# Kernel tuning notes

Measured on AMD Instinct MI355X. Metric: run time of the kernel, lower is better.

Reference implementation:

```python
import jax, jax.numpy as jnp
import numpy as np

B, S, D = 4, 4096, 64

def setup_inputs() -> dict:
    key = jax.random.key(0)
    k1, k2, k3 = jax.random.split(key, 3)
    inputs = jax.random.normal(k1, (B, S, D), dtype=jnp.float32)
    rotation = jax.random.normal(k2, (D, D), dtype=jnp.float32)
    entangle = jax.random.normal(k3, (D, D), dtype=jnp.float32)
    return {"inputs": inputs, "rotation": rotation, "entangle": entangle}

def reference(inputs, rotation, entangle):
    # query/key projections: [B,S,D] @ [D,D] -> [B,S,D]
    query = jnp.einsum('bsd,de->bse', inputs, rotation)
    key = jnp.einsum('bsd,de->bse', inputs, entangle)
    scale = 1.0 / jnp.sqrt(jnp.float32(inputs.shape[-1]))
    # scores: [B,S,S] softmax over last axis
    scores = jax.nn.softmax(jnp.einsum('bqd,bkd->bqk', query, key) * scale, axis=-1)
    # values are the raw inputs (no value projection)
    return jnp.einsum('bqk,bkd->bqd', scores, inputs)
```

## Files before the change

kernel.cpp:

```cpp
#include <hip/hip_runtime.h>
#include <hip/hip_fp16.h>

#define BB 4
#define SS 4096
#define DD 64
#define NSPLIT 8
#define KT_PER (SS / 64 / NSPLIT)

typedef _Float16 half8 __attribute__((ext_vector_type(8)));
typedef _Float16 half4 __attribute__((ext_vector_type(4)));
typedef __fp16 fp16x2 __attribute__((ext_vector_type(2)));
typedef float floatx4 __attribute__((ext_vector_type(4)));

__global__ __launch_bounds__(256) void proj_kernel(
    const float* __restrict__ X, const float* __restrict__ R, const float* __restrict__ E,
    _Float16* __restrict__ Qhi, _Float16* __restrict__ Qlo,
    _Float16* __restrict__ Khi, _Float16* __restrict__ Klo,
    _Float16* __restrict__ Vt)
{
    __shared__ float Rs[64][64];
    __shared__ float Es[64][64];
    __shared__ float Xs[16][68];
    int t = threadIdx.x;
    long rowbase = (long)blockIdx.x * 16;

    for (int j = 0; j < 4; ++j) {
        int idx = j * 256 + t;
        int r = idx >> 4;
        int c = (idx & 15) * 4;
        *(float4*)&Rs[r][c] = ((const float4*)R)[idx];
        *(float4*)&Es[r][c] = ((const float4*)E)[idx];
    }
    *(float4*)&Xs[t >> 4][(t & 15) * 4] = ((const float4*)(X + rowbase * 64))[t];
    __syncthreads();

    int row = t >> 4;
    int c0 = (t & 15) * 4;
    float q[4] = {0.f, 0.f, 0.f, 0.f}, k[4] = {0.f, 0.f, 0.f, 0.f};
#pragma unroll 4
    for (int d = 0; d < 64; ++d) {
        float x = Xs[row][d];
        float4 rv = *(const float4*)&Rs[d][c0];
        float4 ev = *(const float4*)&Es[d][c0];
        q[0] = fmaf(x, rv.x, q[0]); q[1] = fmaf(x, rv.y, q[1]);
        q[2] = fmaf(x, rv.z, q[2]); q[3] = fmaf(x, rv.w, q[3]);
        k[0] = fmaf(x, ev.x, k[0]); k[1] = fmaf(x, ev.y, k[1]);
        k[2] = fmaf(x, ev.z, k[2]); k[3] = fmaf(x, ev.w, k[3]);
    }
    long gq = (rowbase + row) * 64 + c0;
    half4 qh, ql, kh, kl;
#pragma unroll
    for (int j = 0; j < 4; ++j) {
        _Float16 h = (_Float16)q[j];
        qh[j] = h; ql[j] = (_Float16)(q[j] - (float)h);
        h = (_Float16)k[j];
        kh[j] = h; kl[j] = (_Float16)(k[j] - (float)h);
    }
    *(half4*)(Qhi + gq) = qh; *(half4*)(Qlo + gq) = ql;
    *(half4*)(Khi + gq) = kh; *(half4*)(Klo + gq) = kl;

    int d = t >> 2;
    int si = (t & 3) * 4;
    int b = (int)(rowbase >> 12);
    int sbase = (int)(rowbase & 4095);
    half4 v;
#pragma unroll
    for (int j = 0; j < 4; ++j) v[j] = (_Float16)Xs[si + j][d];
    *(half4*)(Vt + ((long)(b * 64 + d)) * SS + sbase + si) = v;
}

#define L2E 1.44269504088896340736f

__device__ __forceinline__ void glds16(const _Float16* g, _Float16* l) {
    __builtin_amdgcn_global_load_lds(
        (const __attribute__((address_space(1))) unsigned*)g,
        (__attribute__((address_space(3))) unsigned*)l, 16, 0, 0);
}

__global__ __launch_bounds__(128, 3) void attn_partial(
    const _Float16* __restrict__ Qhi, const _Float16* __restrict__ Qlo,
    const _Float16* __restrict__ Khi, const _Float16* __restrict__ Klo,
    const _Float16* __restrict__ Vt,
    float* __restrict__ Op, float* __restrict__ Mp, float* __restrict__ Lp)
{
    __shared__ _Float16 Ksh[64 * 64];
    __shared__ _Float16 Ksl[64 * 64];
    __shared__ _Float16 Ps[2 * 32 * 64];

    int t = threadIdx.x;
    int wave = t >> 6;
    int lane = t & 63;
    int l15 = lane & 15;
    int quad = lane >> 4;
    int split = blockIdx.y;
    int b = blockIdx.z;
    int q0 = blockIdx.x * 64 + wave * 32;

    half8 qah0, qah1, qbh0, qbh1, qal0, qal1, qbl0, qbl1;
    {
        long qrow = ((long)b * SS + q0 + l15) * DD;
        qah0 = *(const half8*)(Qhi + qrow + quad * 8);
        qah1 = *(const half8*)(Qhi + qrow + 32 + quad * 8);
        qal0 = *(const half8*)(Qlo + qrow + quad * 8);
        qal1 = *(const half8*)(Qlo + qrow + 32 + quad * 8);
        long qrow2 = qrow + 16 * DD;
        qbh0 = *(const half8*)(Qhi + qrow2 + quad * 8);
        qbh1 = *(const half8*)(Qhi + qrow2 + 32 + quad * 8);
        qbl0 = *(const half8*)(Qlo + qrow2 + quad * 8);
        qbl1 = *(const half8*)(Qlo + qrow2 + 32 + quad * 8);
    }

    floatx4 o[2][4];
#pragma unroll
    for (int qh = 0; qh < 2; ++qh)
#pragma unroll
        for (int i = 0; i < 4; ++i) o[qh][i] = (floatx4){0.f, 0.f, 0.f, 0.f};
    float m_q[2] = {-1e30f, -1e30f};
    float l_q[2] = {0.f, 0.f};

    const float scale = 0.125f * L2E;

    int grow = lane >> 3;
    int gblk = (lane & 7) ^ grow;
    int rm = l15 & 7;
    int p0h = ((quad ^ rm) << 3);

    int kt = split * KT_PER;
    for (int i = 0; i < KT_PER; ++i, ++kt) {
        __syncthreads();
        {
            long ktile = ((long)b * SS + (long)kt * 64) * DD;
            const _Float16* khs = Khi + ktile;
            const _Float16* kls = Klo + ktile;
#pragma unroll
            for (int j = 0; j < 4; ++j) {
                int c = wave * 4 + j;
                int row = c * 8 + grow;
                long goff = (long)row * 64 + gblk * 8;
                glds16(khs + goff, &Ksh[c * 512]);
                glds16(kls + goff, &Ksl[c * 512]);
            }
        }
        __syncthreads();

        half8 vb[4][2];
#pragma unroll
        for (int dt = 0; dt < 4; ++dt)
#pragma unroll
            for (int h = 0; h < 2; ++h)
                vb[dt][h] = *(const half8*)(Vt + ((long)(b * 64 + dt * 16 + l15)) * SS
                                            + kt * 64 + h * 32 + quad * 8);

        floatx4 s[2][4];
#pragma unroll
        for (int ct = 0; ct < 4; ++ct) {
            int rowb = (ct * 16 + l15) * 64;
            half8 ka0h = *(const half8*)&Ksh[rowb + p0h];
            half8 ka1h = *(const half8*)&Ksh[rowb + (p0h ^ 32)];
            half8 ka0l = *(const half8*)&Ksl[rowb + p0h];
            half8 ka1l = *(const half8*)&Ksl[rowb + (p0h ^ 32)];
            floatx4 acc0 = {0.f, 0.f, 0.f, 0.f};
            acc0 = __builtin_amdgcn_mfma_f32_16x16x32_f16(ka0h, qah0, acc0, 0, 0, 0);
            acc0 = __builtin_amdgcn_mfma_f32_16x16x32_f16(ka1h, qah1, acc0, 0, 0, 0);
            acc0 = __builtin_amdgcn_mfma_f32_16x16x32_f16(ka0h, qal0, acc0, 0, 0, 0);
            acc0 = __builtin_amdgcn_mfma_f32_16x16x32_f16(ka1h, qal1, acc0, 0, 0, 0);
            acc0 = __builtin_amdgcn_mfma_f32_16x16x32_f16(ka0l, qah0, acc0, 0, 0, 0);
            acc0 = __builtin_amdgcn_mfma_f32_16x16x32_f16(ka1l, qah1, acc0, 0, 0, 0);
            s[0][ct] = acc0;
            floatx4 acc1 = {0.f, 0.f, 0.f, 0.f};
            acc1 = __builtin_amdgcn_mfma_f32_16x16x32_f16(ka0h, qbh0, acc1, 0, 0, 0);
            acc1 = __builtin_amdgcn_mfma_f32_16x16x32_f16(ka1h, qbh1, acc1, 0, 0, 0);
            acc1 = __builtin_amdgcn_mfma_f32_16x16x32_f16(ka0h, qbl0, acc1, 0, 0, 0);
            acc1 = __builtin_amdgcn_mfma_f32_16x16x32_f16(ka1h, qbl1, acc1, 0, 0, 0);
            acc1 = __builtin_amdgcn_mfma_f32_16x16x32_f16(ka0l, qbh0, acc1, 0, 0, 0);
            acc1 = __builtin_amdgcn_mfma_f32_16x16x32_f16(ka1l, qbh1, acc1, 0, 0, 0);
            s[1][ct] = acc1;
        }

#pragma unroll
        for (int qh = 0; qh < 2; ++qh) {
            float mt = s[qh][0][0];
#pragma unroll
            for (int ct = 0; ct < 4; ++ct)
#pragma unroll
                for (int r = 0; r < 4; ++r)
                    mt = fmaxf(mt, s[qh][ct][r]);
            mt = fmaxf(mt, __shfl_xor(mt, 16));
            mt = fmaxf(mt, __shfl_xor(mt, 32));
            mt *= scale;
            float mn = fmaxf(m_q[qh], mt);
            float alpha = exp2f(m_q[qh] - mn);
            m_q[qh] = mn;

            int prow = (wave * 32 + qh * 16 + l15) * 64;
            float rs = 0.f;
#pragma unroll
            for (int ct = 0; ct < 4; ++ct) {
                float p0 = exp2f(s[qh][ct][0] * scale - mn);
                float p1 = exp2f(s[qh][ct][1] * scale - mn);
                float p2 = exp2f(s[qh][ct][2] * scale - mn);
                float p3 = exp2f(s[qh][ct][3] * scale - mn);
                rs += (p0 + p1) + (p2 + p3);
                union { fp16x2 h2[2]; half4 h4; } u;
                u.h2[0] = __builtin_amdgcn_cvt_pkrtz(p0, p1);
                u.h2[1] = __builtin_amdgcn_cvt_pkrtz(p2, p3);
                int blk = (2 * ct + (quad >> 1)) ^ rm;
                *(half4*)&Ps[prow + blk * 8 + (quad & 1) * 4] = u.h4;
            }
            rs += __shfl_xor(rs, 16);
            rs += __shfl_xor(rs, 32);
            l_q[qh] = l_q[qh] * alpha + rs;

#pragma unroll
            for (int r = 0; r < 4; ++r) {
                float a = __shfl(alpha, quad * 4 + r);
                o[qh][0][r] *= a; o[qh][1][r] *= a;
                o[qh][2][r] *= a; o[qh][3][r] *= a;
            }
        }

#pragma unroll
        for (int h = 0; h < 2; ++h) {
            int pblk = ((4 * h + quad) ^ rm) << 3;
            half8 pa0 = *(const half8*)&Ps[(wave * 32 + l15) * 64 + pblk];
            half8 pa1 = *(const half8*)&Ps[(wave * 32 + 16 + l15) * 64 + pblk];
#pragma unroll
            for (int dt = 0; dt < 4; ++dt) {
                o[0][dt] = __builtin_amdgcn_mfma_f32_16x16x32_f16(pa0, vb[dt][h], o[0][dt], 0, 0, 0);
                o[1][dt] = __builtin_amdgcn_mfma_f32_16x16x32_f16(pa1, vb[dt][h], o[1][dt], 0, 0, 0);
            }
        }
    }

    long pbase = ((long)b * NSPLIT + split) * SS;
#pragma unroll
    for (int qh = 0; qh < 2; ++qh) {
#pragma unroll
        for (int r = 0; r < 4; ++r) {
            int q = q0 + qh * 16 + quad * 4 + r;
            long orow = (pbase + q) * DD;
#pragma unroll
            for (int dt = 0; dt < 4; ++dt)
                Op[orow + dt * 16 + l15] = o[qh][dt][r];
        }
    }
    if (quad == 0) {
        Mp[pbase + q0 + l15] = m_q[0];
        Lp[pbase + q0 + l15] = l_q[0];
        Mp[pbase + q0 + 16 + l15] = m_q[1];
        Lp[pbase + q0 + 16 + l15] = l_q[1];
    }
}

__global__ __launch_bounds__(256) void combine_kernel(
    const float* __restrict__ Op, const float* __restrict__ Mp,
    const float* __restrict__ Lp, float* __restrict__ Out)
{
    int t = threadIdx.x;
    int qi = t >> 4;
    int d4 = (t & 15) * 4;
    long gq = (long)blockIdx.x * 16 + qi;
    int b = (int)(gq >> 12);
    int s = (int)(gq & 4095);

    float m = -1e30f;
    for (int i = 0; i < NSPLIT; ++i)
        m = fmaxf(m, Mp[((long)b * NSPLIT + i) * SS + s]);
    float l = 0.f;
    float4 o = {0.f, 0.f, 0.f, 0.f};
    for (int i = 0; i < NSPLIT; ++i) {
        long pb = ((long)b * NSPLIT + i) * SS + s;
        float a = exp2f(Mp[pb] - m);
        l = fmaf(Lp[pb], a, l);
        float4 oi = *(const float4*)(Op + pb * DD + d4);
        o.x = fmaf(oi.x, a, o.x); o.y = fmaf(oi.y, a, o.y);
        o.z = fmaf(oi.z, a, o.z); o.w = fmaf(oi.w, a, o.w);
    }
    float inv = 1.f / l;
    float4 r = {o.x * inv, o.y * inv, o.z * inv, o.w * inv};
    *(float4*)(Out + gq * DD + d4) = r;
}

extern "C" void kernel_launch(void* const* d_in, const int* in_sizes, int n_in,
                              void* d_out, int out_size, void* d_ws, size_t ws_size,
                              hipStream_t stream) {
    const float* X = (const float*)d_in[0];
    const float* R = (const float*)d_in[1];
    const float* E = (const float*)d_in[2];
    float* Out = (float*)d_out;

    const size_t N = (size_t)BB * SS * DD;
    _Float16* Qhi = (_Float16*)d_ws;
    _Float16* Qlo = Qhi + N;
    _Float16* Khi = Qlo + N;
    _Float16* Klo = Khi + N;
    _Float16* Vt  = Klo + N;
    float* Op = (float*)(Vt + N);
    float* Mp = Op + (size_t)BB * NSPLIT * SS * DD;
    float* Lp = Mp + (size_t)BB * NSPLIT * SS;

    proj_kernel<<<dim3(BB * SS / 16), 256, 0, stream>>>(X, R, E, Qhi, Qlo, Khi, Klo, Vt);
    attn_partial<<<dim3(SS / 64, NSPLIT, BB), 128, 0, stream>>>(Qhi, Qlo, Khi, Klo, Vt, Op, Mp, Lp);
    combine_kernel<<<dim3(BB * SS / 16), 256, 0, stream>>>(Op, Mp, Lp, Out);
}
```

Measured before the change: 138.4 us.

## Double-buffer K tiles in LDS with async prefetch and halve key splits

The attention kernel now holds two LDS buffers for the hi/lo K tiles. It issues the global-to-LDS loads for the next tile while the current tile is being computed, which drops one barrier per iteration and hides load latency. The number of key-dimension splits drops from 8 to 4, so each block walks twice as many tiles, there are fewer partial results to combine, and the grid has half as many blocks. The extra LDS use lowers the occupancy hint from 3 to 2 blocks per CU, which trades parallelism for overlap.

```diff
diff --git a/kernel.cpp b/kernel.cpp
--- a/kernel.cpp
+++ b/kernel.cpp
@@ -4,7 +4,7 @@
 #define BB 4
 #define SS 4096
 #define DD 64
-#define NSPLIT 8
+#define NSPLIT 4
 #define KT_PER (SS / 64 / NSPLIT)
 
 typedef _Float16 half8 __attribute__((ext_vector_type(8)));
@@ -77,14 +77,14 @@
         (__attribute__((address_space(3))) unsigned*)l, 16, 0, 0);
 }
 
-__global__ __launch_bounds__(128, 3) void attn_partial(
+__global__ __launch_bounds__(128, 2) void attn_partial(
     const _Float16* __restrict__ Qhi, const _Float16* __restrict__ Qlo,
     const _Float16* __restrict__ Khi, const _Float16* __restrict__ Klo,
     const _Float16* __restrict__ Vt,
     float* __restrict__ Op, float* __restrict__ Mp, float* __restrict__ Lp)
 {
-    __shared__ _Float16 Ksh[64 * 64];
-    __shared__ _Float16 Ksl[64 * 64];
+    __shared__ _Float16 Ksh[2][64 * 64];
+    __shared__ _Float16 Ksl[2][64 * 64];
     __shared__ _Float16 Ps[2 * 32 * 64];
 
     int t = threadIdx.x;
@@ -125,22 +125,21 @@
     int rm = l15 & 7;
     int p0h = ((quad ^ rm) << 3);
 
-    int kt = split * KT_PER;
-    for (int i = 0; i < KT_PER; ++i, ++kt) {
-        __syncthreads();
-        {
-            long ktile = ((long)b * SS + (long)kt * 64) * DD;
-            const _Float16* khs = Khi + ktile;
-            const _Float16* kls = Klo + ktile;
-#pragma unroll
-            for (int j = 0; j < 4; ++j) {
-                int c = wave * 4 + j;
-                int row = c * 8 + grow;
-                long goff = (long)row * 64 + gblk * 8;
-                glds16(khs + goff, &Ksh[c * 512]);
-                glds16(kls + goff, &Ksl[c * 512]);
-            }
-        }
+    int kt0 = split * KT_PER;
+    const _Float16* khs_base = Khi + ((long)b * SS + (long)kt0 * 64) * DD;
+    const _Float16* kls_base = Klo + ((long)b * SS + (long)kt0 * 64) * DD;
+
+#pragma unroll
+    for (int j = 0; j < 4; ++j) {
+        int c = wave * 4 + j;
+        long goff = (long)(c * 8 + grow) * 64 + gblk * 8;
+        glds16(khs_base + goff, &Ksh[0][c * 512]);
+        glds16(kls_base + goff, &Ksl[0][c * 512]);
+    }
+
+    for (int i = 0; i < KT_PER; ++i) {
+        int kt = kt0 + i;
+        int buf = i & 1;
         __syncthreads();
 
         half8 vb[4][2];
@@ -151,14 +150,25 @@
                 vb[dt][h] = *(const half8*)(Vt + ((long)(b * 64 + dt * 16 + l15)) * SS
                                             + kt * 64 + h * 32 + quad * 8);
 
+        if (i + 1 < KT_PER) {
+            long tbase = (long)(i + 1) * 64 * DD;
+#pragma unroll
+            for (int j = 0; j < 4; ++j) {
+                int c = wave * 4 + j;
+                long goff = tbase + (long)(c * 8 + grow) * 64 + gblk * 8;
+                glds16(khs_base + goff, &Ksh[buf ^ 1][c * 512]);
+                glds16(kls_base + goff, &Ksl[buf ^ 1][c * 512]);
+            }
+        }
+
         floatx4 s[2][4];
 #pragma unroll
         for (int ct = 0; ct < 4; ++ct) {
             int rowb = (ct * 16 + l15) * 64;
-            half8 ka0h = *(const half8*)&Ksh[rowb + p0h];
-            half8 ka1h = *(const half8*)&Ksh[rowb + (p0h ^ 32)];
-            half8 ka0l = *(const half8*)&Ksl[rowb + p0h];
-            half8 ka1l = *(const half8*)&Ksl[rowb + (p0h ^ 32)];
+            half8 ka0h = *(const half8*)&Ksh[buf][rowb + p0h];
+            half8 ka1h = *(const half8*)&Ksh[buf][rowb + (p0h ^ 32)];
+            half8 ka0l = *(const half8*)&Ksl[buf][rowb + p0h];
+            half8 ka1l = *(const half8*)&Ksl[buf][rowb + (p0h ^ 32)];
             floatx4 acc0 = {0.f, 0.f, 0.f, 0.f};
             acc0 = __builtin_amdgcn_mfma_f32_16x16x32_f16(ka0h, qah0, acc0, 0, 0, 0);
             acc0 = __builtin_amdgcn_mfma_f32_16x16x32_f16(ka1h, qah1, acc0, 0, 0, 0);
```

New measurement: 125.1 us. -9.6%, faster.
